# Kernel optimization log

Measured on AMD Instinct MI355X. Metric: run time of the kernel, lower is better.

The kernel has to match this reference:

```python
import jax, jax.numpy as jnp
import numpy as np

B, T, D, H = 4, 2048, 768, 12
DH = D // H  # 64
SCALE = float(DH) ** 0.5  # NOTE: original code MULTIPLIES by sqrt(d_head)


def setup_inputs() -> dict:
    key = jax.random.key(0)
    k1, k2, k3 = jax.random.split(key, 3)
    x = jax.random.normal(k1, (B, T, D), dtype=jnp.float32)
    w_qkv = jax.random.normal(k2, (3 * D, D), dtype=jnp.float32) * (D ** -0.5)
    w_out = jax.random.normal(k3, (D, D), dtype=jnp.float32) * (D ** -0.5)
    return {"x": x, "w_qkv": w_qkv, "w_out": w_out}


def reference(x, w_qkv, w_out):
    b, t, d = x.shape
    # qkv_layer: Linear(d, 3d, bias=False) -> x @ W.T
    qkv = jnp.einsum('btd,ed->bte', x, w_qkv)  # [b, t, 3d]
    # rearrange 'b t (d k h) -> k b h t d' with k=3, h=H: split as (DH, 3, H)
    qkv = qkv.reshape(b, t, DH, 3, H)
    qkv = jnp.transpose(qkv, (3, 0, 4, 1, 2))  # [3, b, h, t, dh]
    q, k, v = qkv[0], qkv[1], qkv[2]
    # energy multiplied (faithfully) by sqrt(d_head)
    energy = jnp.einsum('bhid,bhjd->bhij', q, k) * SCALE
    attn = jax.nn.softmax(energy, axis=-1)
    o = jnp.einsum('bhij,bhjd->bhid', attn, v)  # [b, h, t, dh]
    # rearrange 'b h t d -> b t (h d)'
    o = jnp.transpose(o, (0, 2, 1, 3)).reshape(b, t, d)
    return jnp.einsum('btd,ed->bte', o, w_out)
```

## Files before the change

kernel.cpp:

```cpp
#include <hip/hip_runtime.h>
#include <hip/hip_bf16.h>
#include <cstdint>
#include <cstddef>

#define Bsz 4
#define Tsz 2048
#define Dsz 768
#define Hsz 12
#define DHsz 64
#define Msz (Bsz * Tsz)

typedef __attribute__((ext_vector_type(8))) short short8;
typedef __attribute__((ext_vector_type(4))) float floatx4;

typedef const __attribute__((address_space(1))) unsigned int* gas1;
typedef __attribute__((address_space(3))) unsigned int* las3;
__device__ __forceinline__ void dma16(const unsigned short* g, unsigned short* l) {
  __builtin_amdgcn_global_load_lds((gas1)g, (las3)l, 16, 0, 0);
}

__device__ __forceinline__ unsigned short f2bf(float f) {
  union { float f; unsigned u; } v; v.f = f;
  unsigned u = v.u;
  unsigned r = u + 0x7fffu + ((u >> 16) & 1u);
  return (unsigned short)(r >> 16);
}
__device__ __forceinline__ float bf2f(unsigned short h) {
  union { unsigned u; float f; } v; v.u = ((unsigned)h) << 16; return v.f;
}
__device__ __forceinline__ unsigned pk_bf2(float a, float b) {
  union { __hip_bfloat162 b2; unsigned u; } cv;
  cv.b2 = __float22bfloat162_rn(make_float2(a, b));
  return cv.u;
}

#define TREAD(arr, row, s) \
  (*reinterpret_cast<const short8*>(&(arr)[((row) << 6) + ((((s) * 4 + quad) ^ ((row) & 7)) << 3)]))

__global__ void split_x(const float* __restrict__ src,
                        unsigned short* __restrict__ hi,
                        unsigned short* __restrict__ lo) {
  int i = (blockIdx.x * blockDim.x + threadIdx.x) * 4;
  float4 v = *reinterpret_cast<const float4*>(src + i);
  ushort4 h, l;
  h.x = f2bf(v.x); l.x = f2bf(v.x - bf2f(h.x));
  h.y = f2bf(v.y); l.y = f2bf(v.y - bf2f(h.y));
  h.z = f2bf(v.z); l.z = f2bf(v.z - bf2f(h.z));
  h.w = f2bf(v.w); l.w = f2bf(v.w - bf2f(h.w));
  *reinterpret_cast<ushort4*>(hi + i) = h;
  *reinterpret_cast<ushort4*>(lo + i) = l;
}

__global__ void split_w(const float* __restrict__ src,
                        unsigned short* __restrict__ hi,
                        unsigned short* __restrict__ lo) {
  int i = (blockIdx.x * blockDim.x + threadIdx.x) * 4;
  int rp = i / Dsz, c = i % Dsz;
  int kk = rp / Dsz;
  int rem = rp - kk * Dsz;
  int h = rem >> 6, d = rem & 63;
  const float* s = src + (size_t)(d * 36 + kk * 12 + h) * Dsz + c;
  float4 v = *reinterpret_cast<const float4*>(s);
  ushort4 hh, ll;
  hh.x = f2bf(v.x); ll.x = f2bf(v.x - bf2f(hh.x));
  hh.y = f2bf(v.y); ll.y = f2bf(v.y - bf2f(hh.y));
  hh.z = f2bf(v.z); ll.z = f2bf(v.z - bf2f(hh.z));
  hh.w = f2bf(v.w); ll.w = f2bf(v.w - bf2f(hh.w));
  *reinterpret_cast<ushort4*>(hi + i) = hh;
  *reinterpret_cast<ushort4*>(lo + i) = ll;
}

__global__ void cvt_f32_bf16(const float* __restrict__ src,
                             unsigned short* __restrict__ dst, int n) {
  int i = (blockIdx.x * blockDim.x + threadIdx.x) * 4;
  int stride = gridDim.x * blockDim.x * 4;
  for (; i < n; i += stride) {
    float4 v = *reinterpret_cast<const float4*>(src + i);
    ushort4 o;
    o.x = f2bf(v.x); o.y = f2bf(v.y); o.z = f2bf(v.z); o.w = f2bf(v.w);
    *reinterpret_cast<ushort4*>(dst + i) = o;
  }
}

__launch_bounds__(256, 3)
__global__ void gemm_qkv(const unsigned short* __restrict__ xh,
                         const unsigned short* __restrict__ xl,
                         const unsigned short* __restrict__ wh,
                         const unsigned short* __restrict__ wl,
                         unsigned short* __restrict__ Qhp,
                         unsigned short* __restrict__ Qlp,
                         unsigned short* __restrict__ Khp,
                         unsigned short* __restrict__ Klp,
                         unsigned short* __restrict__ Vtp) {
  __shared__ unsigned short Ah[128 * 64], Al[128 * 64];
  __shared__ unsigned short Bh[64 * 64],  Bl[64 * 64];
  const int mt128 = blockIdx.x;
  const int nblk = blockIdx.y;
  const int kk = nblk / 12;
  const int h  = nblk % 12;
  const int tid = threadIdx.x;
  const int w = tid >> 6, lane = tid & 63, l16 = lane & 15, quad = lane >> 4;
  const int lrow = lane >> 3;
  const int lgl  = (lane & 7) ^ lrow;

  floatx4 acc[2][4];
#pragma unroll
  for (int mt = 0; mt < 2; ++mt)
#pragma unroll
    for (int nt = 0; nt < 4; ++nt) acc[mt][nt] = (floatx4){0.f, 0.f, 0.f, 0.f};

  const size_t abase = (size_t)(mt128 * 128) * Dsz;
  const size_t bbase = (size_t)(kk * Dsz + h * 64) * Dsz;

  for (int kc = 0; kc < Dsz; kc += 64) {
    __syncthreads();
#pragma unroll
    for (int j = 0; j < 4; ++j) {
      const int R0 = w * 32 + j * 8;
      const size_t g = abase + (size_t)(R0 + lrow) * Dsz + kc + lgl * 8;
      dma16(xh + g, &Ah[R0 * 64]);
      if (kk != 2) dma16(xl + g, &Al[R0 * 64]);
    }
#pragma unroll
    for (int j = 0; j < 2; ++j) {
      const int R0 = w * 16 + j * 8;
      const size_t g = bbase + (size_t)(R0 + lrow) * Dsz + kc + lgl * 8;
      dma16(wh + g, &Bh[R0 * 64]);
      if (kk != 2) dma16(wl + g, &Bl[R0 * 64]);
    }
    __syncthreads();
#pragma unroll
    for (int s = 0; s < 2; ++s) {
      short8 ah[2], al[2];
#pragma unroll
      for (int mt = 0; mt < 2; ++mt) ah[mt] = TREAD(Ah, w * 32 + mt * 16 + l16, s);
      if (kk != 2) {
#pragma unroll
        for (int mt = 0; mt < 2; ++mt) al[mt] = TREAD(Al, w * 32 + mt * 16 + l16, s);
      }
#pragma unroll
      for (int nt = 0; nt < 4; ++nt) {
        short8 bh = TREAD(Bh, nt * 16 + l16, s);
#pragma unroll
        for (int mt = 0; mt < 2; ++mt)
          acc[mt][nt] = __builtin_amdgcn_mfma_f32_16x16x32_bf16(ah[mt], bh, acc[mt][nt], 0, 0, 0);
        if (kk != 2) {
          short8 bl = TREAD(Bl, nt * 16 + l16, s);
#pragma unroll
          for (int mt = 0; mt < 2; ++mt) {
            acc[mt][nt] = __builtin_amdgcn_mfma_f32_16x16x32_bf16(ah[mt], bl, acc[mt][nt], 0, 0, 0);
            acc[mt][nt] = __builtin_amdgcn_mfma_f32_16x16x32_bf16(al[mt], bh, acc[mt][nt], 0, 0, 0);
          }
        }
      }
    }
  }
#pragma unroll
  for (int mt = 0; mt < 2; ++mt) {
    const int mbase = mt128 * 128 + w * 32 + mt * 16 + quad * 4;
    const int b = mbase >> 11;
    const size_t hoff = (size_t)(b * Hsz + h) * Tsz * DHsz;
    const int t0 = mbase & (Tsz - 1);
    if (kk == 2) {
      unsigned short* dst = Vtp + hoff;
#pragma unroll
      for (int nt = 0; nt < 4; ++nt) {
        int d = nt * 16 + l16;
        uint2 pk;
        pk.x = pk_bf2(acc[mt][nt][0], acc[mt][nt][1]);
        pk.y = pk_bf2(acc[mt][nt][2], acc[mt][nt][3]);
        *reinterpret_cast<uint2*>(&dst[(size_t)d * Tsz + t0]) = pk;
      }
    } else {
      const float sc = (kk == 0) ? 8.0f : 1.0f;
      unsigned short* dh_ = ((kk == 0) ? Qhp : Khp) + hoff;
      unsigned short* dl_ = ((kk == 0) ? Qlp : Klp) + hoff;
#pragma unroll
      for (int nt = 0; nt < 4; ++nt) {
        int d = nt * 16 + l16;
#pragma unroll
        for (int r = 0; r < 4; ++r) {
          float v = acc[mt][nt][r] * sc;
          unsigned short hv = f2bf(v);
          dh_[(size_t)(t0 + r) * DHsz + d] = hv;
          dl_[(size_t)(t0 + r) * DHsz + d] = f2bf(v - bf2f(hv));
        }
      }
    }
  }
}

__launch_bounds__(256, 3)
__global__ void attn(const unsigned short* __restrict__ Qhp,
                     const unsigned short* __restrict__ Qlp,
                     const unsigned short* __restrict__ Khp,
                     const unsigned short* __restrict__ Klp,
                     const unsigned short* __restrict__ Vtp,
                     unsigned short* __restrict__ Ob) {
  __shared__ unsigned short Ksh[64 * 64], Ksl[64 * 64], Vs[64 * 64];
  __shared__ unsigned short plT[4][2][16][68];
  const int bid = blockIdx.x;
  const int xcd = bid & 7, slot = bid >> 3;
  const int bh = xcd * 6 + (slot >> 4);
  const int qt = slot & 15;
  const int tid = threadIdx.x;
  const int w = tid >> 6, lane = tid & 63, l16 = lane & 15, quad = lane >> 4;
  const int lrow = lane >> 3;
  const int lgl  = (lane & 7) ^ lrow;
  const size_t hoff = (size_t)bh * Tsz * DHsz;
  const unsigned short* Kh = Khp + hoff;
  const unsigned short* Kl = Klp + hoff;
  const unsigned short* Vt = Vtp + hoff;

  short8 qh[2][2], ql[2][2];
#pragma unroll
  for (int mt = 0; mt < 2; ++mt) {
    const size_t qoff = hoff + (size_t)(qt * 128 + w * 32 + mt * 16 + l16) * DHsz + quad * 8;
    qh[mt][0] = *reinterpret_cast<const short8*>(Qhp + qoff);
    qh[mt][1] = *reinterpret_cast<const short8*>(Qhp + qoff + 32);
    ql[mt][0] = *reinterpret_cast<const short8*>(Qlp + qoff);
    ql[mt][1] = *reinterpret_cast<const short8*>(Qlp + qoff + 32);
  }

  floatx4 Of[2][4];
#pragma unroll
  for (int mt = 0; mt < 2; ++mt)
#pragma unroll
    for (int nt = 0; nt < 4; ++nt) Of[mt][nt] = (floatx4){0.f, 0.f, 0.f, 0.f};
  float m_i[2] = {-1e30f, -1e30f};
  float l_i[2] = {0.f, 0.f};

  for (int kt = 0; kt < Tsz; kt += 64) {
    __syncthreads();
#pragma unroll
    for (int j = 0; j < 2; ++j) {
      const int R0 = w * 16 + j * 8;
      dma16(Kh + (size_t)(kt + R0 + lrow) * DHsz + lgl * 8, &Ksh[R0 * 64]);
      dma16(Kl + (size_t)(kt + R0 + lrow) * DHsz + lgl * 8, &Ksl[R0 * 64]);
      dma16(Vt + (size_t)(R0 + lrow) * Tsz + kt + lgl * 8,  &Vs[R0 * 64]);
    }
    __syncthreads();

    floatx4 S[2][4];
#pragma unroll
    for (int mt = 0; mt < 2; ++mt)
#pragma unroll
      for (int nt = 0; nt < 4; ++nt) S[mt][nt] = (floatx4){0.f, 0.f, 0.f, 0.f};
#pragma unroll
    for (int s = 0; s < 2; ++s) {
#pragma unroll
      for (int nt = 0; nt < 4; ++nt) {
        short8 kf_h = TREAD(Ksh, nt * 16 + l16, s);
        short8 kf_l = TREAD(Ksl, nt * 16 + l16, s);
        S[0][nt] = __builtin_amdgcn_mfma_f32_16x16x32_bf16(kf_h, qh[0][s], S[0][nt], 0, 0, 0);
        S[0][nt] = __builtin_amdgcn_mfma_f32_16x16x32_bf16(kf_l, qh[0][s], S[0][nt], 0, 0, 0);
        S[0][nt] = __builtin_amdgcn_mfma_f32_16x16x32_bf16(kf_h, ql[0][s], S[0][nt], 0, 0, 0);
        S[1][nt] = __builtin_amdgcn_mfma_f32_16x16x32_bf16(kf_h, qh[1][s], S[1][nt], 0, 0, 0);
        S[1][nt] = __builtin_amdgcn_mfma_f32_16x16x32_bf16(kf_l, qh[1][s], S[1][nt], 0, 0, 0);
        S[1][nt] = __builtin_amdgcn_mfma_f32_16x16x32_bf16(kf_h, ql[1][s], S[1][nt], 0, 0, 0);
      }
    }

#pragma unroll
    for (int mt = 0; mt < 2; ++mt) {
      float mx = -1e30f;
#pragma unroll
      for (int nt = 0; nt < 4; ++nt)
#pragma unroll
        for (int r = 0; r < 4; ++r) mx = fmaxf(mx, S[mt][nt][r]);
      mx = fmaxf(mx, __shfl_xor(mx, 16));
      mx = fmaxf(mx, __shfl_xor(mx, 32));
      float mnew = fmaxf(m_i[mt], mx);
      float alpha = __expf(m_i[mt] - mnew);
      m_i[mt] = mnew;
      float ls = 0.f;
#pragma unroll
      for (int nt = 0; nt < 4; ++nt) {
        float p0 = __expf(S[mt][nt][0] - mnew);
        float p1 = __expf(S[mt][nt][1] - mnew);
        float p2 = __expf(S[mt][nt][2] - mnew);
        float p3 = __expf(S[mt][nt][3] - mnew);
        ls += (p0 + p1) + (p2 + p3);
        uint2 pk;
        pk.x = pk_bf2(p0, p1);
        pk.y = pk_bf2(p2, p3);
        *reinterpret_cast<uint2*>(&plT[w][mt][l16][nt * 16 + quad * 4]) = pk;
      }
      l_i[mt] = l_i[mt] * alpha + ls;
#pragma unroll
      for (int nt = 0; nt < 4; ++nt) {
        Of[mt][nt][0] *= alpha; Of[mt][nt][1] *= alpha;
        Of[mt][nt][2] *= alpha; Of[mt][nt][3] *= alpha;
      }
    }

    short8 pf[2][2];
#pragma unroll
    for (int s = 0; s < 2; ++s) {
      pf[0][s] = *reinterpret_cast<const short8*>(&plT[w][0][l16][s * 32 + quad * 8]);
      pf[1][s] = *reinterpret_cast<const short8*>(&plT[w][1][l16][s * 32 + quad * 8]);
    }
#pragma unroll
    for (int nt = 0; nt < 4; ++nt) {
#pragma unroll
      for (int s = 0; s < 2; ++s) {
        short8 vf = TREAD(Vs, nt * 16 + l16, s);
        Of[0][nt] = __builtin_amdgcn_mfma_f32_16x16x32_bf16(vf, pf[0][s], Of[0][nt], 0, 0, 0);
        Of[1][nt] = __builtin_amdgcn_mfma_f32_16x16x32_bf16(vf, pf[1][s], Of[1][nt], 0, 0, 0);
      }
    }
  }

  const int b = bh / Hsz, h = bh % Hsz;
#pragma unroll
  for (int mt = 0; mt < 2; ++mt) {
    float ls = l_i[mt];
    ls += __shfl_xor(ls, 16);
    ls += __shfl_xor(ls, 32);
    float inv = 1.0f / ls;
    int t = qt * 128 + w * 32 + mt * 16 + l16;
    unsigned short* orow = Ob + (size_t)(b * Tsz + t) * Dsz + h * DHsz;
#pragma unroll
    for (int nt = 0; nt < 4; ++nt) {
      uint2 pk;
      pk.x = pk_bf2(Of[mt][nt][0] * inv, Of[mt][nt][1] * inv);
      pk.y = pk_bf2(Of[mt][nt][2] * inv, Of[mt][nt][3] * inv);
      *reinterpret_cast<uint2*>(&orow[nt * 16 + quad * 4]) = pk;
    }
  }
}

__launch_bounds__(256, 3)
__global__ void gemm_out(const unsigned short* __restrict__ ob,
                         const unsigned short* __restrict__ wb,
                         float* __restrict__ out) {
  __shared__ unsigned short As[128 * 64];
  __shared__ unsigned short Bs[64 * 64];
  const int mt128 = blockIdx.x;
  const int n0 = blockIdx.y * 64;
  const int tid = threadIdx.x;
  const int w = tid >> 6, lane = tid & 63, l16 = lane & 15, quad = lane >> 4;
  const int lrow = lane >> 3;
  const int lgl  = (lane & 7) ^ lrow;

  floatx4 acc[2][4];
#pragma unroll
  for (int mt = 0; mt < 2; ++mt)
#pragma unroll
    for (int nt = 0; nt < 4; ++nt) acc[mt][nt] = (floatx4){0.f, 0.f, 0.f, 0.f};

  const size_t abase = (size_t)(mt128 * 128) * Dsz;
  const size_t bbase = (size_t)n0 * Dsz;

  for (int kc = 0; kc < Dsz; kc += 64) {
    __syncthreads();
#pragma unroll
    for (int j = 0; j < 4; ++j) {
      const int R0 = w * 32 + j * 8;
      dma16(ob + abase + (size_t)(R0 + lrow) * Dsz + kc + lgl * 8, &As[R0 * 64]);
    }
#pragma unroll
    for (int j = 0; j < 2; ++j) {
      const int R0 = w * 16 + j * 8;
      dma16(wb + bbase + (size_t)(R0 + lrow) * Dsz + kc + lgl * 8, &Bs[R0 * 64]);
    }
    __syncthreads();
#pragma unroll
    for (int s = 0; s < 2; ++s) {
      short8 a[2];
#pragma unroll
      for (int mt = 0; mt < 2; ++mt) a[mt] = TREAD(As, w * 32 + mt * 16 + l16, s);
#pragma unroll
      for (int nt = 0; nt < 4; ++nt) {
        short8 b = TREAD(Bs, nt * 16 + l16, s);
#pragma unroll
        for (int mt = 0; mt < 2; ++mt)
          acc[mt][nt] = __builtin_amdgcn_mfma_f32_16x16x32_bf16(a[mt], b, acc[mt][nt], 0, 0, 0);
      }
    }
  }
#pragma unroll
  for (int mt = 0; mt < 2; ++mt) {
    const int mbase = mt128 * 128 + w * 32 + mt * 16 + quad * 4;
#pragma unroll
    for (int nt = 0; nt < 4; ++nt) {
      int n = n0 + nt * 16 + l16;
#pragma unroll
      for (int r = 0; r < 4; ++r) {
        out[(size_t)(mbase + r) * Dsz + n] = acc[mt][nt][r];
      }
    }
  }
}

extern "C" void kernel_launch(void* const* d_in, const int* in_sizes, int n_in,
                              void* d_out, int out_size, void* d_ws, size_t ws_size,
                              hipStream_t stream) {
  const float* x     = (const float*)d_in[0];
  const float* w_qkv = (const float*)d_in[1];
  const float* w_out = (const float*)d_in[2];
  float* out = (float*)d_out;

  unsigned short* ws = (unsigned short*)d_ws;
  const size_t nX  = (size_t)Msz * Dsz;
  const size_t nWq = (size_t)3 * Dsz * Dsz;
  const size_t nWo = (size_t)Dsz * Dsz;
  const size_t nHd = (size_t)Bsz * Hsz * Tsz * DHsz;

  unsigned short* xh  = ws;
  unsigned short* xl  = xh + nX;
  unsigned short* wh  = xl + nX;
  unsigned short* wl  = wh + nWq;
  unsigned short* wob = wl + nWq;
  unsigned short* Qhp = wob + nWo;
  unsigned short* Qlp = Qhp + nHd;
  unsigned short* Khp = Qlp + nHd;
  unsigned short* Klp = Khp + nHd;
  unsigned short* Vtp = Klp + nHd;
  unsigned short* Ob  = xh;

  split_x<<<nX / 4 / 256, 256, 0, stream>>>(x, xh, xl);
  split_w<<<nWq / 4 / 256, 256, 0, stream>>>(w_qkv, wh, wl);
  cvt_f32_bf16<<<256, 256, 0, stream>>>(w_out, wob, (int)nWo);
  gemm_qkv<<<dim3(64, 36), 256, 0, stream>>>(xh, xl, wh, wl, Qhp, Qlp, Khp, Klp, Vtp);
  attn<<<768, 256, 0, stream>>>(Qhp, Qlp, Khp, Klp, Vtp, Ob);
  gemm_out<<<dim3(64, 12), 256, 0, stream>>>(Ob, wob, out);
}
```

Baseline: 295.9 us.

## Concatenate hi/lo splits along K, widen GEMM N-tiles, fold log2e into Q

The hi and lo bf16 parts of x and w_qkv are now stored interleaved in rows twice as wide. The QKV GEMM runs as one concatenated K loop that computes xh·wh + xh·wl + xl·wh, using 128-wide N tiles, one LDS buffer per operand and a single MFMA per step. The output GEMM also moves to 128-wide N tiles for more operand reuse. Q is pre-scaled by sqrt(d_head)*log2(e), so the softmax can use the hardware exp2 instead of __expf. The cost is that the V projection now also does the three-term split-precision work it used to skip, and the grids have fewer, larger blocks, which may leave CUs underused.

```diff
diff --git a/kernel.cpp b/kernel.cpp
--- a/kernel.cpp
+++ b/kernel.cpp
@@ -9,9 +9,18 @@
 #define Hsz 12
 #define DHsz 64
 #define Msz (Bsz * Tsz)
+#define K2 1536
+#define K3 2304
+#define QSCALE 11.5415603f
 
 typedef __attribute__((ext_vector_type(8))) short short8;
 typedef __attribute__((ext_vector_type(4))) float floatx4;
+
+#if __has_builtin(__builtin_amdgcn_exp2f)
+#define EXP2(x) __builtin_amdgcn_exp2f(x)
+#else
+#define EXP2(x) exp2f(x)
+#endif
 
 typedef const __attribute__((address_space(1))) unsigned int* gas1;
 typedef __attribute__((address_space(3))) unsigned int* las3;
@@ -38,22 +47,22 @@
   (*reinterpret_cast<const short8*>(&(arr)[((row) << 6) + ((((s) * 4 + quad) ^ ((row) & 7)) << 3)]))
 
 __global__ void split_x(const float* __restrict__ src,
-                        unsigned short* __restrict__ hi,
-                        unsigned short* __restrict__ lo) {
+                        unsigned short* __restrict__ dst) {
   int i = (blockIdx.x * blockDim.x + threadIdx.x) * 4;
+  int row = i / Dsz, col = i % Dsz;
   float4 v = *reinterpret_cast<const float4*>(src + i);
   ushort4 h, l;
   h.x = f2bf(v.x); l.x = f2bf(v.x - bf2f(h.x));
   h.y = f2bf(v.y); l.y = f2bf(v.y - bf2f(h.y));
   h.z = f2bf(v.z); l.z = f2bf(v.z - bf2f(h.z));
   h.w = f2bf(v.w); l.w = f2bf(v.w - bf2f(h.w));
-  *reinterpret_cast<ushort4*>(hi + i) = h;
-  *reinterpret_cast<ushort4*>(lo + i) = l;
+  unsigned short* base = dst + (size_t)row * K2 + col;
+  *reinterpret_cast<ushort4*>(base) = h;
+  *reinterpret_cast<ushort4*>(base + Dsz) = l;
 }
 
 __global__ void split_w(const float* __restrict__ src,
-                        unsigned short* __restrict__ hi,
-                        unsigned short* __restrict__ lo) {
+                        unsigned short* __restrict__ dst) {
   int i = (blockIdx.x * blockDim.x + threadIdx.x) * 4;
   int rp = i / Dsz, c = i % Dsz;
   int kk = rp / Dsz;
@@ -66,8 +75,9 @@
   hh.y = f2bf(v.y); ll.y = f2bf(v.y - bf2f(hh.y));
   hh.z = f2bf(v.z); ll.z = f2bf(v.z - bf2f(hh.z));
   hh.w = f2bf(v.w); ll.w = f2bf(v.w - bf2f(hh.w));
-  *reinterpret_cast<ushort4*>(hi + i) = hh;
-  *reinterpret_cast<ushort4*>(lo + i) = ll;
+  unsigned short* base = dst + (size_t)rp * K2 + c;
+  *reinterpret_cast<ushort4*>(base) = hh;
+  *reinterpret_cast<ushort4*>(base + Dsz) = ll;
 }
 
 __global__ void cvt_f32_bf16(const float* __restrict__ src,
@@ -83,107 +93,86 @@
 }
 
 __launch_bounds__(256, 3)
-__global__ void gemm_qkv(const unsigned short* __restrict__ xh,
-                         const unsigned short* __restrict__ xl,
-                         const unsigned short* __restrict__ wh,
-                         const unsigned short* __restrict__ wl,
+__global__ void gemm_qkv(const unsigned short* __restrict__ xs,
+                         const unsigned short* __restrict__ wsb,
                          unsigned short* __restrict__ Qhp,
                          unsigned short* __restrict__ Qlp,
                          unsigned short* __restrict__ Khp,
                          unsigned short* __restrict__ Klp,
                          unsigned short* __restrict__ Vtp) {
-  __shared__ unsigned short Ah[128 * 64], Al[128 * 64];
-  __shared__ unsigned short Bh[64 * 64],  Bl[64 * 64];
+  __shared__ unsigned short As[128 * 64], Bs[128 * 64];
   const int mt128 = blockIdx.x;
   const int nblk = blockIdx.y;
-  const int kk = nblk / 12;
-  const int h  = nblk % 12;
   const int tid = threadIdx.x;
   const int w = tid >> 6, lane = tid & 63, l16 = lane & 15, quad = lane >> 4;
   const int lrow = lane >> 3;
   const int lgl  = (lane & 7) ^ lrow;
 
-  floatx4 acc[2][4];
+  floatx4 acc[2][8];
 #pragma unroll
   for (int mt = 0; mt < 2; ++mt)
 #pragma unroll
-    for (int nt = 0; nt < 4; ++nt) acc[mt][nt] = (floatx4){0.f, 0.f, 0.f, 0.f};
-
-  const size_t abase = (size_t)(mt128 * 128) * Dsz;
-  const size_t bbase = (size_t)(kk * Dsz + h * 64) * Dsz;
-
-  for (int kc = 0; kc < Dsz; kc += 64) {
+    for (int nt = 0; nt < 8; ++nt) acc[mt][nt] = (floatx4){0.f, 0.f, 0.f, 0.f};
+
+  const size_t abase = (size_t)(mt128 * 128) * K2;
+  const size_t bbase = (size_t)(nblk * 128) * K2;
+
+  for (int kc = 0; kc < K3; kc += 64) {
+    const int akc = (kc < 768)  ? kc : kc - 768;
+    const int bkc = (kc < 1536) ? kc : kc - 1536;
     __syncthreads();
 #pragma unroll
     for (int j = 0; j < 4; ++j) {
       const int R0 = w * 32 + j * 8;
-      const size_t g = abase + (size_t)(R0 + lrow) * Dsz + kc + lgl * 8;
-      dma16(xh + g, &Ah[R0 * 64]);
-      if (kk != 2) dma16(xl + g, &Al[R0 * 64]);
-    }
-#pragma unroll
-    for (int j = 0; j < 2; ++j) {
-      const int R0 = w * 16 + j * 8;
-      const size_t g = bbase + (size_t)(R0 + lrow) * Dsz + kc + lgl * 8;
-      dma16(wh + g, &Bh[R0 * 64]);
-      if (kk != 2) dma16(wl + g, &Bl[R0 * 64]);
+      dma16(xs + abase + (size_t)(R0 + lrow) * K2 + akc + lgl * 8, &As[R0 * 64]);
+    }
+#pragma unroll
+    for (int j = 0; j < 4; ++j) {
+      const int R0 = w * 32 + j * 8;
+      dma16(wsb + bbase + (size_t)(R0 + lrow) * K2 + bkc + lgl * 8, &Bs[R0 * 64]);
     }
     __syncthreads();
 #pragma unroll
     for (int s = 0; s < 2; ++s) {
-      short8 ah[2], al[2];
-#pragma unroll
-      for (int mt = 0; mt < 2; ++mt) ah[mt] = TREAD(Ah, w * 32 + mt * 16 + l16, s);
-      if (kk != 2) {
-#pragma unroll
-        for (int mt = 0; mt < 2; ++mt) al[mt] = TREAD(Al, w * 32 + mt * 16 + l16, s);
-      }
-#pragma unroll
-      for (int nt = 0; nt < 4; ++nt) {
-        short8 bh = TREAD(Bh, nt * 16 + l16, s);
+      short8 a[2];
+#pragma unroll
+      for (int mt = 0; mt < 2; ++mt) a[mt] = TREAD(As, w * 32 + mt * 16 + l16, s);
+#pragma unroll
+      for (int nt = 0; nt < 8; ++nt) {
+        short8 b = TREAD(Bs, nt * 16 + l16, s);
 #pragma unroll
         for (int mt = 0; mt < 2; ++mt)
-          acc[mt][nt] = __builtin_amdgcn_mfma_f32_16x16x32_bf16(ah[mt], bh, acc[mt][nt], 0, 0, 0);
-        if (kk != 2) {
-          short8 bl = TREAD(Bl, nt * 16 + l16, s);
-#pragma unroll
-          for (int mt = 0; mt < 2; ++mt) {
-            acc[mt][nt] = __builtin_amdgcn_mfma_f32_16x16x32_bf16(ah[mt], bl, acc[mt][nt], 0, 0, 0);
-            acc[mt][nt] = __builtin_amdgcn_mfma_f32_16x16x32_bf16(al[mt], bh, acc[mt][nt], 0, 0, 0);
-          }
-        }
-      }
-    }
-  }
+          acc[mt][nt] = __builtin_amdgcn_mfma_f32_16x16x32_bf16(a[mt], b, acc[mt][nt], 0, 0, 0);
+      }
+    }
+  }
+  const int kk = nblk / 6;
+  const int h0 = (nblk % 6) * 2;
+  unsigned short* dh_ = (kk == 0) ? Qhp : Khp;
+  unsigned short* dl_ = (kk == 0) ? Qlp : Klp;
+  const float sc = (kk == 0) ? QSCALE : 1.0f;
 #pragma unroll
   for (int mt = 0; mt < 2; ++mt) {
     const int mbase = mt128 * 128 + w * 32 + mt * 16 + quad * 4;
     const int b = mbase >> 11;
-    const size_t hoff = (size_t)(b * Hsz + h) * Tsz * DHsz;
     const int t0 = mbase & (Tsz - 1);
-    if (kk == 2) {
-      unsigned short* dst = Vtp + hoff;
-#pragma unroll
-      for (int nt = 0; nt < 4; ++nt) {
-        int d = nt * 16 + l16;
+#pragma unroll
+    for (int nt = 0; nt < 8; ++nt) {
+      const int h = h0 + (nt >> 2);
+      const int d = (nt & 3) * 16 + l16;
+      const size_t hoff = (size_t)(b * Hsz + h) * Tsz * DHsz;
+      if (kk == 2) {
         uint2 pk;
         pk.x = pk_bf2(acc[mt][nt][0], acc[mt][nt][1]);
         pk.y = pk_bf2(acc[mt][nt][2], acc[mt][nt][3]);
-        *reinterpret_cast<uint2*>(&dst[(size_t)d * Tsz + t0]) = pk;
-      }
-    } else {
-      const float sc = (kk == 0) ? 8.0f : 1.0f;
-      unsigned short* dh_ = ((kk == 0) ? Qhp : Khp) + hoff;
-      unsigned short* dl_ = ((kk == 0) ? Qlp : Klp) + hoff;
-#pragma unroll
-      for (int nt = 0; nt < 4; ++nt) {
-        int d = nt * 16 + l16;
+        *reinterpret_cast<uint2*>(&Vtp[hoff + (size_t)d * Tsz + t0]) = pk;
+      } else {
 #pragma unroll
         for (int r = 0; r < 4; ++r) {
           float v = acc[mt][nt][r] * sc;
           unsigned short hv = f2bf(v);
-          dh_[(size_t)(t0 + r) * DHsz + d] = hv;
-          dl_[(size_t)(t0 + r) * DHsz + d] = f2bf(v - bf2f(hv));
+          dh_[hoff + (size_t)(t0 + r) * DHsz + d] = hv;
+          dl_[hoff + (size_t)(t0 + r) * DHsz + d] = f2bf(v - bf2f(hv));
         }
       }
     }
@@ -271,15 +260,15 @@
       mx = fmaxf(mx, __shfl_xor(mx, 16));
       mx = fmaxf(mx, __shfl_xor(mx, 32));
       float mnew = fmaxf(m_i[mt], mx);
-      float alpha = __expf(m_i[mt] - mnew);
+      float alpha = EXP2(m_i[mt] - mnew);
       m_i[mt] = mnew;
       float ls = 0.f;
 #pragma unroll
       for (int nt = 0; nt < 4; ++nt) {
-        float p0 = __expf(S[mt][nt][0] - mnew);
-        float p1 = __expf(S[mt][nt][1] - mnew);
-        float p2 = __expf(S[mt][nt][2] - mnew);
-        float p3 = __expf(S[mt][nt][3] - mnew);
+        float p0 = EXP2(S[mt][nt][0] - mnew);
+        float p1 = EXP2(S[mt][nt][1] - mnew);
+        float p2 = EXP2(S[mt][nt][2] - mnew);
+        float p3 = EXP2(S[mt][nt][3] - mnew);
         ls += (p0 + p1) + (p2 + p3);
         uint2 pk;
         pk.x = pk_bf2(p0, p1);
@@ -335,19 +324,19 @@
                          const unsigned short* __restrict__ wb,
                          float* __restrict__ out) {
   __shared__ unsigned short As[128 * 64];
-  __shared__ unsigned short Bs[64 * 64];
+  __shared__ unsigned short Bs[128 * 64];
   const int mt128 = blockIdx.x;
-  const int n0 = blockIdx.y * 64;
+  const int n0 = blockIdx.y * 128;
   const int tid = threadIdx.x;
   const int w = tid >> 6, lane = tid & 63, l16 = lane & 15, quad = lane >> 4;
   const int lrow = lane >> 3;
   const int lgl  = (lane & 7) ^ lrow;
 
-  floatx4 acc[2][4];
+  floatx4 acc[2][8];
 #pragma unroll
   for (int mt = 0; mt < 2; ++mt)
 #pragma unroll
-    for (int nt = 0; nt < 4; ++nt) acc[mt][nt] = (floatx4){0.f, 0.f, 0.f, 0.f};
+    for (int nt = 0; nt < 8; ++nt) acc[mt][nt] = (floatx4){0.f, 0.f, 0.f, 0.f};
 
   const size_t abase = (size_t)(mt128 * 128) * Dsz;
   const size_t bbase = (size_t)n0 * Dsz;
@@ -360,8 +349,8 @@
       dma16(ob + abase + (size_t)(R0 + lrow) * Dsz + kc + lgl * 8, &As[R0 * 64]);
     }
 #pragma unroll
-    for (int j = 0; j < 2; ++j) {
-      const int R0 = w * 16 + j * 8;
+    for (int j = 0; j < 4; ++j) {
+      const int R0 = w * 32 + j * 8;
       dma16(wb + bbase + (size_t)(R0 + lrow) * Dsz + kc + lgl * 8, &Bs[R0 * 64]);
     }
     __syncthreads();
@@ -371,7 +360,7 @@
 #pragma unroll
       for (int mt = 0; mt < 2; ++mt) a[mt] = TREAD(As, w * 32 + mt * 16 + l16, s);
 #pragma unroll
-      for (int nt = 0; nt < 4; ++nt) {
+      for (int nt = 0; nt < 8; ++nt) {
         short8 b = TREAD(Bs, nt * 16 + l16, s);
 #pragma unroll
         for (int mt = 0; mt < 2; ++mt)
@@ -383,7 +372,7 @@
   for (int mt = 0; mt < 2; ++mt) {
     const int mbase = mt128 * 128 + w * 32 + mt * 16 + quad * 4;
 #pragma unroll
-    for (int nt = 0; nt < 4; ++nt) {
+    for (int nt = 0; nt < 8; ++nt) {
       int n = n0 + nt * 16 + l16;
 #pragma unroll
       for (int r = 0; r < 4; ++r) {
@@ -402,27 +391,25 @@
   float* out = (float*)d_out;
 
   unsigned short* ws = (unsigned short*)d_ws;
-  const size_t nX  = (size_t)Msz * Dsz;
-  const size_t nWq = (size_t)3 * Dsz * Dsz;
+  const size_t nXs = (size_t)Msz * K2;
+  const size_t nWs = (size_t)3 * Dsz * K2;
   const size_t nWo = (size_t)Dsz * Dsz;
   const size_t nHd = (size_t)Bsz * Hsz * Tsz * DHsz;
 
-  unsigned short* xh  = ws;
-  unsigned short* xl  = xh + nX;
-  unsigned short* wh  = xl + nX;
-  unsigned short* wl  = wh + nWq;
-  unsigned short* wob = wl + nWq;
+  unsigned short* xs  = ws;
+  unsigned short* wsb = xs + nXs;
+  unsigned short* wob = wsb + nWs;
   unsigned short* Qhp = wob + nWo;
   unsigned short* Qlp = Qhp + nHd;
   unsigned short* Khp = Qlp + nHd;
   unsigned short* Klp = Khp + nHd;
   unsigned short* Vtp = Klp + nHd;
-  unsigned short* Ob  = xh;
-
-  split_x<<<nX / 4 / 256, 256, 0, stream>>>(x, xh, xl);
-  split_w<<<nWq / 4 / 256, 256, 0, stream>>>(w_qkv, wh, wl);
+  unsigned short* Ob  = xs;
+
+  split_x<<<(int)(nXs / 2 / 1024), 256, 0, stream>>>(x, xs);
+  split_w<<<(int)(nWs / 2 / 1024), 256, 0, stream>>>(w_qkv, wsb);
   cvt_f32_bf16<<<256, 256, 0, stream>>>(w_out, wob, (int)nWo);
-  gemm_qkv<<<dim3(64, 36), 256, 0, stream>>>(xh, xl, wh, wl, Qhp, Qlp, Khp, Klp, Vtp);
+  gemm_qkv<<<dim3(64, 18), 256, 0, stream>>>(xs, wsb, Qhp, Qlp, Khp, Klp, Vtp);
   attn<<<768, 256, 0, stream>>>(Qhp, Qlp, Khp, Klp, Vtp, Ob);
-  gemm_out<<<dim3(64, 12), 256, 0, stream>>>(Ob, wob, out);
-}
+  gemm_out<<<dim3(64, 6), 256, 0, stream>>>(Ob, wob, out);
+}
```

Measured after the change: 327.7 us. 10.7% more time.
